# Performance work log

Measured on AMD Instinct MI355X. Metric: run time of the kernel, lower is better.

The kernel has to match this reference:

```python
import jax, jax.numpy as jnp
import numpy as np

B, SQ, SKV, E, H = 4, 2048, 2048, 1024, 16
HD = E // H  # 64


def stablemax(x):
    # StableMax: s(x) = x+1 if x>=0 else 1/(1-x), normalized along last axis
    s = jnp.where(x >= 0, x + 1.0, 1.0 / (1.0 - x))
    return s / jnp.sum(s, axis=-1, keepdims=True)


def setup_inputs() -> dict:
    key = jax.random.key(0)
    ks = jax.random.split(key, 6)
    scale = 1.0 / np.sqrt(E)
    return {
        "query": jax.random.normal(ks[0], (B, SQ, E), jnp.float32),
        "key_value": jax.random.normal(ks[1], (B, SKV, E), jnp.float32),
        "Wq": jax.random.normal(ks[2], (E, E), jnp.float32) * scale,
        "bq": jnp.zeros((E,), jnp.float32),
        "Wk": jax.random.normal(ks[3], (E, E), jnp.float32) * scale,
        "bk": jnp.zeros((E,), jnp.float32),
        "Wv": jax.random.normal(ks[4], (E, E), jnp.float32) * scale,
        "bv": jnp.zeros((E,), jnp.float32),
        "Wo": jax.random.normal(ks[5], (E, E), jnp.float32) * scale,
        "bo": jnp.zeros((E,), jnp.float32),
    }


def reference(query, key_value, Wq, bq, Wk, bk, Wv, bv, Wo, bo):
    b = query.shape[0]
    # linear projections (torch Linear: x @ W^T + b)
    q = query @ Wq.T + bq
    k = key_value @ Wk.T + bk
    v = key_value @ Wv.T + bv
    # [B, H, S, HD]
    q = q.reshape(b, -1, H, HD).transpose(0, 2, 1, 3)
    k = k.reshape(b, -1, H, HD).transpose(0, 2, 1, 3)
    v = v.reshape(b, -1, H, HD).transpose(0, 2, 1, 3)
    scores = jnp.einsum("bhqd,bhkd->bhqk", q, k) / np.sqrt(HD).astype(np.float32)
    attn = stablemax(scores)  # dropout is identity in eval mode
    context = jnp.einsum("bhqk,bhkd->bhqd", attn, v)
    context = context.transpose(0, 2, 1, 3).reshape(b, -1, E)
    return context @ Wo.T + bo
```

## Files before the change

kernel.cpp:

```cpp
#include <hip/hip_runtime.h>

typedef __bf16 bf16;
typedef __bf16 bf16x8 __attribute__((ext_vector_type(8)));
typedef __bf16 bf16x4 __attribute__((ext_vector_type(4)));
typedef _Float16 f16;
typedef _Float16 f16x2 __attribute__((ext_vector_type(2)));
typedef _Float16 f16x4 __attribute__((ext_vector_type(4)));
typedef _Float16 f16x8 __attribute__((ext_vector_type(8)));
typedef float f32x4 __attribute__((ext_vector_type(4)));

__device__ __forceinline__ f32x4 mfma_qk(bf16x8 a, bf16x8 b, f32x4 c) {
    return __builtin_amdgcn_mfma_f32_16x16x32_bf16(a, b, c, 0, 0, 0);
}
__device__ __forceinline__ f32x4 mfma_pv32(f16x8 a, f16x8 b, f32x4 c) {
    return __builtin_amdgcn_mfma_f32_16x16x32_f16(a, b, c, 0, 0, 0);
}

#define GLOAD_LDS16(gp, lp)                                                    \
    __builtin_amdgcn_global_load_lds(                                          \
        (const __attribute__((address_space(1))) unsigned int*)(gp),           \
        (__attribute__((address_space(3))) unsigned int*)(lp), 16, 0, 0)

__global__ __launch_bounds__(256) void cast_inputs(
    const float* __restrict__ w0, const float* __restrict__ w1,
    const float* __restrict__ w2, const float* __restrict__ w3,
    const float* __restrict__ kv, const float* __restrict__ q,
    bf16* __restrict__ Wb, bf16* __restrict__ KVa, bf16* __restrict__ Qb) {
    long i4 = (long)blockIdx.x * 256 + threadIdx.x;
    const float* src;
    bf16* dst;
    long loc;
    if (i4 < 1048576) {
        int which = (int)(i4 >> 18);
        loc = (i4 & 262143) << 2;
        src = which == 0 ? w0 : which == 1 ? w1 : which == 2 ? w2 : w3;
        dst = Wb + ((long)which << 20);
    } else if (i4 < 3145728) {
        loc = (i4 - 1048576) << 2;
        src = kv; dst = KVa;
    } else {
        loc = (i4 - 3145728) << 2;
        src = q; dst = Qb;
    }
    float4 f = *(const float4*)(src + loc);
    bf16x4 o;
    o[0] = (bf16)f.x; o[1] = (bf16)f.y; o[2] = (bf16)f.z; o[3] = (bf16)f.w;
    *(bf16x4*)(dst + loc) = o;
}

__device__ __forceinline__ void gemm_core(
    const bf16* __restrict__ A, const bf16* __restrict__ Wt,
    const float* __restrict__ bias, void* __restrict__ Yv,
    const int om, bf16* smem, const int n0, const int m0) {
    constexpr int Kd = 1024, Nd = 1024;
    constexpr int TP = 132;
    bf16* As = smem;
    bf16* Bs = smem + 8192;
    const int tid = threadIdx.x;
    const int wid = tid >> 6, lane = tid & 63;
    const int l16 = lane & 15, quad = lane >> 4;
    const int mh = (wid >> 1) * 64, nh = (wid & 1) * 64;

    f32x4 acc[4][4];
#pragma unroll
    for (int i = 0; i < 4; ++i)
#pragma unroll
        for (int j = 0; j < 4; ++j) acc[i][j] = (f32x4){0.f, 0.f, 0.f, 0.f};

    for (int k0 = 0; k0 < Kd; k0 += 64) {
#pragma unroll
        for (int j = 0; j < 4; ++j) {
            const int s = j * 256 + tid;
            const int r = s >> 3, c8 = (s & 7) ^ (r & 7);
            GLOAD_LDS16(A + (long)(m0 + r) * Kd + k0 + c8 * 8, &As[s * 8]);
            GLOAD_LDS16(Wt + (long)(n0 + r) * Kd + k0 + c8 * 8, &Bs[s * 8]);
        }
        __syncthreads();
#pragma unroll
        for (int kc = 0; kc < 2; ++kc) {
            bf16x8 af[4], bq[4];
#pragma unroll
            for (int i = 0; i < 4; ++i) {
                const int row = mh + i * 16 + l16;
                af[i] = *(const bf16x8*)&As[(row * 8 + ((kc * 4 + quad) ^ (row & 7))) * 8];
            }
#pragma unroll
            for (int i = 0; i < 4; ++i) {
                const int row = nh + i * 16 + l16;
                bq[i] = *(const bf16x8*)&Bs[(row * 8 + ((kc * 4 + quad) ^ (row & 7))) * 8];
            }
#pragma unroll
            for (int i = 0; i < 4; ++i)
#pragma unroll
                for (int j = 0; j < 4; ++j)
                    acc[i][j] = mfma_qk(af[i], bq[j], acc[i][j]);
        }
        __syncthreads();
    }

    if (om == 2) {
#pragma unroll
        for (int j = 0; j < 4; ++j) {
            const int col = nh + j * 16 + l16;
            const float bv = bias[n0 + col];
#pragma unroll
            for (int i = 0; i < 4; ++i)
#pragma unroll
                for (int p = 0; p < 2; ++p) {
                    f16x2 pk2;
                    pk2[0] = (f16)(acc[i][j][p * 2 + 0] + bv);
                    pk2[1] = (f16)(acc[i][j][p * 2 + 1] + bv);
                    *(f16x2*)&smem[col * TP + mh + i * 16 + quad * 4 + p * 2] = pk2;
                }
        }
        __syncthreads();
        const int b_ = m0 >> 11, skv0 = m0 & 2047;
        const int rowc = tid & 15;
        const int B32 = (rowc >> 2) * 32, g4 = (rowc & 3) * 4;
        const f16* sm = (const f16*)smem;
#pragma unroll
        for (int c = 0; c < 8; ++c) {
            const int col = (tid >> 4) + c * 16;
            const int colg = n0 + col;
            f16x4 lo = *(const f16x4*)&sm[col * TP + B32 + g4];
            f16x4 hi = *(const f16x4*)&sm[col * TP + B32 + 16 + g4];
            f16x8 v = __builtin_shufflevector(lo, hi, 0, 1, 2, 3, 4, 5, 6, 7);
            const long base = ((long)((b_ * 16 + (colg >> 6)) * 64 + (colg & 63))) << 11;
            *(f16x8*)((f16*)Yv + base + skv0 + rowc * 8) = v;
        }
    } else {
#pragma unroll
        for (int j = 0; j < 4; ++j) {
            const int col = n0 + nh + j * 16 + l16;
            const float bv = bias[col];
#pragma unroll
            for (int i = 0; i < 4; ++i)
#pragma unroll
                for (int r = 0; r < 4; ++r) {
                    int row = m0 + mh + i * 16 + quad * 4 + r;
                    float v = acc[i][j][r] + bv;
                    if (om == 1)
                        ((float*)Yv)[(long)row * Nd + col] = v;
                    else
                        ((bf16*)Yv)[(long)row * Nd + col] = (bf16)v;
                }
        }
    }
}

__global__ __launch_bounds__(256) void proj_qkv(
    const bf16* __restrict__ Qb, const bf16* __restrict__ KVa,
    const bf16* __restrict__ Wb,
    const float* __restrict__ bq, const float* __restrict__ bk,
    const float* __restrict__ bv,
    bf16* __restrict__ Qw, bf16* __restrict__ Kw, f16* __restrict__ Vt) {
    __shared__ __align__(16) bf16 smem[16896];
    const int lin = blockIdx.x + (blockIdx.y << 3) + (blockIdx.z << 9);
    const int nid = (lin & 7) * 192 + (lin >> 3);
    const int z = nid >> 9, rem = nid & 511;
    const int n0 = (rem & 7) << 7, m0 = (rem >> 3) << 7;
    if (z == 0)
        gemm_core(Qb, Wb, bq, Qw, 0, smem, n0, m0);
    else if (z == 1)
        gemm_core(KVa, Wb + (1l << 20), bk, Kw, 0, smem, n0, m0);
    else
        gemm_core(KVa, Wb + (2l << 20), bv, Vt, 2, smem, n0, m0);
}

__global__ __launch_bounds__(256) void gemm_o(
    const bf16* __restrict__ Cw, const bf16* __restrict__ Wo,
    const float* __restrict__ bo, float* __restrict__ out) {
    __shared__ __align__(16) bf16 smem[16896];
    const int lin = blockIdx.x + (blockIdx.y << 3);
    const int nid = (lin & 7) * 64 + (lin >> 3);
    gemm_core(Cw, Wo, bo, out, 1, smem, (nid & 7) << 7, (nid >> 3) << 7);
}

__global__ __launch_bounds__(256) void attn_kernel(
    const bf16* __restrict__ Q, const bf16* __restrict__ K,
    const f16* __restrict__ Vt, bf16* __restrict__ C) {
    constexpr int E = 1024, S = 2048, KVB = 64;
    __shared__ __align__(16) char smem_raw[32768];
    bf16* Ks0 = (bf16*)smem_raw;
    bf16* Ks1 = (bf16*)(smem_raw + 8192);
    f16* Vt0 = (f16*)(smem_raw + 16384);
    f16* Vt1 = (f16*)(smem_raw + 24576);

    const int tid = threadIdx.x;
    const int wid = tid >> 6, lane = tid & 63;
    const int l16 = lane & 15, quad = lane >> 4;
    const int lin = blockIdx.x + (blockIdx.y << 4) + (blockIdx.z << 8);
    const int nid = (lin & 7) * 128 + (lin >> 3);
    const int qt = nid & 15, h = (nid >> 4) & 15, b = nid >> 8;

    const long q0 = (long)b * S + qt * 128;
    const bf16* Qg = Q + q0 * E + h * 64;
    const bf16* Kg = K + (long)b * S * E + h * 64;
    const f16* Vg = Vt + ((long)(b * 16 + h) << 17);

    bf16x8 qf[2][2];
#pragma unroll
    for (int mt = 0; mt < 2; ++mt)
#pragma unroll
        for (int kc = 0; kc < 2; ++kc)
            qf[mt][kc] = *(const bf16x8*)(Qg + (long)(wid * 32 + mt * 16 + l16) * E + kc * 32 + quad * 8);

    f16x8 ones8;
#pragma unroll
    for (int j = 0; j < 8; ++j) ones8[j] = (f16)1.0f;

    f32x4 ctx[2][4];
    f32x4 dacc[2];
#pragma unroll
    for (int mt = 0; mt < 2; ++mt) {
        dacc[mt] = (f32x4){0.f, 0.f, 0.f, 0.f};
#pragma unroll
        for (int dt = 0; dt < 4; ++dt) ctx[mt][dt] = (f32x4){0.f, 0.f, 0.f, 0.f};
    }

    auto stage = [&](int kv0, bf16* Kd, f16* Vd) {
#pragma unroll
        for (int j = 0; j < 2; ++j) {
            const int s = j * 256 + tid;
            const int r = s >> 3, c8 = (s & 7) ^ (r & 7);
            GLOAD_LDS16(Kg + (long)(kv0 + r) * E + c8 * 8, &Kd[s * 8]);
        }
#pragma unroll
        for (int j = 0; j < 2; ++j) {
            const int s = j * 256 + tid;
            const int r = s >> 3, c8 = (s & 7) ^ (r & 7);
            GLOAD_LDS16(Vg + (long)r * S + kv0 + c8 * 8, &Vd[s * 8]);
        }
    };

    auto compute = [&](const bf16* Kc, const f16* Vc) {
#pragma unroll
        for (int kvp = 0; kvp < 2; ++kvp) {
            f32x4 sacc[2][2];
#pragma unroll
            for (int sh = 0; sh < 2; ++sh) {
                const int rk = kvp * 32 + sh * 16 + l16, rb = rk & 7;
                bf16x8 kf0 = *(const bf16x8*)&Kc[(rk * 8 + (quad ^ rb)) * 8];
                bf16x8 kf1 = *(const bf16x8*)&Kc[(rk * 8 + ((quad + 4) ^ rb)) * 8];
                __builtin_amdgcn_s_setprio(1);
#pragma unroll
                for (int mt = 0; mt < 2; ++mt) {
                    f32x4 t = mfma_qk(kf0, qf[mt][0], (f32x4){0.f, 0.f, 0.f, 0.f});
                    sacc[sh][mt] = mfma_qk(kf1, qf[mt][1], t);
                }
                __builtin_amdgcn_s_setprio(0);
            }
            f16x8 pp[2];
#pragma unroll
            for (int mt = 0; mt < 2; ++mt)
#pragma unroll
                for (int sh = 0; sh < 2; ++sh)
#pragma unroll
                    for (int r = 0; r < 4; ++r) {
                        float x = sacc[sh][mt][r];
                        float u = __builtin_fmaf(__builtin_fabsf(x), 0.125f, 1.0f);
                        float sv = (x >= 0.f) ? u : __builtin_amdgcn_rcpf(u);
                        pp[mt][sh * 4 + r] = (f16)sv;
                    }
            __builtin_amdgcn_s_setprio(1);
            dacc[0] = mfma_pv32(ones8, pp[0], dacc[0]);
            dacc[1] = mfma_pv32(ones8, pp[1], dacc[1]);
            __builtin_amdgcn_s_setprio(0);
            const int cL = 4 * kvp + quad;
#pragma unroll
            for (int dt = 0; dt < 4; ++dt) {
                const int rv = dt * 16 + l16;
                f16x8 vf = *(const f16x8*)&Vc[(rv * 8 + (cL ^ (rv & 7))) * 8];
                __builtin_amdgcn_s_setprio(1);
#pragma unroll
                for (int mt = 0; mt < 2; ++mt)
                    ctx[mt][dt] = mfma_pv32(vf, pp[mt], ctx[mt][dt]);
                __builtin_amdgcn_s_setprio(0);
            }
        }
    };

    stage(0, Ks0, Vt0);
#pragma unroll 1
    for (int t = 0; t < 31; ++t) {
        const int sel = t & 1;
        stage((t + 1) * KVB, sel ? Ks0 : Ks1, sel ? Vt0 : Vt1);
        asm volatile("s_waitcnt vmcnt(4)\ns_barrier" ::: "memory");
        compute(sel ? Ks1 : Ks0, sel ? Vt1 : Vt0);
        asm volatile("s_waitcnt lgkmcnt(0)\ns_barrier" ::: "memory");
    }
    asm volatile("s_waitcnt vmcnt(0)\ns_barrier" ::: "memory");
    compute(Ks1, Vt1);
    __syncthreads();

    float scl[2];
#pragma unroll
    for (int mt = 0; mt < 2; ++mt) scl[mt] = __builtin_amdgcn_rcpf(dacc[mt][0]);

    bf16* Os = (bf16*)smem_raw;
#pragma unroll
    for (int mt = 0; mt < 2; ++mt)
#pragma unroll
        for (int dt = 0; dt < 4; ++dt) {
            bf16x4 o;
#pragma unroll
            for (int r = 0; r < 4; ++r) o[r] = (bf16)(ctx[mt][dt][r] * scl[mt]);
            *(bf16x4*)&Os[(wid * 32 + mt * 16 + l16) * 68 + dt * 16 + quad * 4] = o;
        }
    __syncthreads();
    {
        const int r = tid >> 1, c = (tid & 1) * 32;
        bf16* cp = C + (q0 + r) * E + h * 64 + c;
#pragma unroll
        for (int j = 0; j < 4; ++j)
            *(bf16x8*)(cp + j * 8) = *(const bf16x8*)&Os[r * 68 + c + j * 8];
    }
}

extern "C" void kernel_launch(void* const* d_in, const int* in_sizes, int n_in,
                              void* d_out, int out_size, void* d_ws, size_t ws_size,
                              hipStream_t stream) {
    const float* query = (const float*)d_in[0];
    const float* keyv  = (const float*)d_in[1];
    const float* Wq = (const float*)d_in[2];
    const float* bq = (const float*)d_in[3];
    const float* Wk = (const float*)d_in[4];
    const float* bk = (const float*)d_in[5];
    const float* Wv = (const float*)d_in[6];
    const float* bv = (const float*)d_in[7];
    const float* Wo = (const float*)d_in[8];
    const float* bo = (const float*)d_in[9];

    char* ws = (char*)d_ws;
    bf16* Wb  = (bf16*)ws;
    bf16* KVa = (bf16*)(ws + (8l << 20));
    bf16* Qb  = (bf16*)(ws + (24l << 20));
    bf16* Qw  = (bf16*)(ws + (40l << 20));
    f16*  Vt  = (f16*)(ws + (56l << 20));
    bf16* Kw  = (bf16*)d_out;
    bf16* Cw  = KVa;

    cast_inputs<<<20480, 256, 0, stream>>>(Wq, Wk, Wv, Wo, keyv, query, Wb, KVa, Qb);

    proj_qkv<<<dim3(8, 64, 3), 256, 0, stream>>>(Qb, KVa, Wb, bq, bk, bv, Qw, Kw, Vt);

    attn_kernel<<<dim3(16, 16, 4), 256, 0, stream>>>(Qw, Kw, Vt, Cw);

    gemm_o<<<dim3(8, 64), 256, 0, stream>>>(Cw, Wb + (3l << 20), bo, (float*)d_out);
}
```

Baseline: 329.5 us.

## Triple-buffer 32-row KV tiles in attention and fold score scale into Wq

The attention main loop changes from double-buffered 64-row K/V tiles to a triple-buffered ring of 32-row tiles. Each stage issues one 16-byte load per thread for K and one for V, and LDS addresses are precomputed per buffer. Only one barrier per step is kept, and each load can be in flight across two compute steps. The 1/sqrt(HD) scale is folded into Wq and bq when casting, which removes the per-score multiply, and the f16 conversion uses packed round-toward-zero conversion. The risks are more barriers per KV element and a slight numerical change from RTZ rounding and the pre-scaled bf16 Wq.

Measured after the change: 312.9 us. -5.1%, faster.

```diff
diff --git a/kernel.cpp b/kernel.cpp
--- a/kernel.cpp
+++ b/kernel.cpp
@@ -7,6 +7,7 @@
 typedef _Float16 f16x2 __attribute__((ext_vector_type(2)));
 typedef _Float16 f16x4 __attribute__((ext_vector_type(4)));
 typedef _Float16 f16x8 __attribute__((ext_vector_type(8)));
+typedef __fp16 h16x2 __attribute__((ext_vector_type(2)));
 typedef float f32x4 __attribute__((ext_vector_type(4)));
 
 __device__ __forceinline__ f32x4 mfma_qk(bf16x8 a, bf16x8 b, f32x4 c) {
@@ -14,6 +15,10 @@
 }
 __device__ __forceinline__ f32x4 mfma_pv32(f16x8 a, f16x8 b, f32x4 c) {
     return __builtin_amdgcn_mfma_f32_16x16x32_f16(a, b, c, 0, 0, 0);
+}
+__device__ __forceinline__ f16x2 pkrtz(float a, float b) {
+    h16x2 r = __builtin_amdgcn_cvt_pkrtz(a, b);
+    return __builtin_bit_cast(f16x2, r);
 }
 
 #define GLOAD_LDS16(gp, lp)                                                    \
@@ -30,11 +35,13 @@
     const float* src;
     bf16* dst;
     long loc;
+    float sc = 1.0f;
     if (i4 < 1048576) {
         int which = (int)(i4 >> 18);
         loc = (i4 & 262143) << 2;
         src = which == 0 ? w0 : which == 1 ? w1 : which == 2 ? w2 : w3;
         dst = Wb + ((long)which << 20);
+        if (which == 0) sc = 0.125f;
     } else if (i4 < 3145728) {
         loc = (i4 - 1048576) << 2;
         src = kv; dst = KVa;
@@ -44,14 +51,15 @@
     }
     float4 f = *(const float4*)(src + loc);
     bf16x4 o;
-    o[0] = (bf16)f.x; o[1] = (bf16)f.y; o[2] = (bf16)f.z; o[3] = (bf16)f.w;
+    o[0] = (bf16)(f.x * sc); o[1] = (bf16)(f.y * sc);
+    o[2] = (bf16)(f.z * sc); o[3] = (bf16)(f.w * sc);
     *(bf16x4*)(dst + loc) = o;
 }
 
 __device__ __forceinline__ void gemm_core(
     const bf16* __restrict__ A, const bf16* __restrict__ Wt,
     const float* __restrict__ bias, void* __restrict__ Yv,
-    const int om, bf16* smem, const int n0, const int m0) {
+    const int om, bf16* smem, const int n0, const int m0, const float bsc) {
     constexpr int Kd = 1024, Nd = 1024;
     constexpr int TP = 132;
     bf16* As = smem;
@@ -102,7 +110,7 @@
 #pragma unroll
         for (int j = 0; j < 4; ++j) {
             const int col = nh + j * 16 + l16;
-            const float bv = bias[n0 + col];
+            const float bv = bias[n0 + col] * bsc;
 #pragma unroll
             for (int i = 0; i < 4; ++i)
 #pragma unroll
@@ -132,7 +140,7 @@
 #pragma unroll
         for (int j = 0; j < 4; ++j) {
             const int col = n0 + nh + j * 16 + l16;
-            const float bv = bias[col];
+            const float bv = bias[col] * bsc;
 #pragma unroll
             for (int i = 0; i < 4; ++i)
 #pragma unroll
@@ -160,11 +168,11 @@
     const int z = nid >> 9, rem = nid & 511;
     const int n0 = (rem & 7) << 7, m0 = (rem >> 3) << 7;
     if (z == 0)
-        gemm_core(Qb, Wb, bq, Qw, 0, smem, n0, m0);
+        gemm_core(Qb, Wb, bq, Qw, 0, smem, n0, m0, 0.125f);
     else if (z == 1)
-        gemm_core(KVa, Wb + (1l << 20), bk, Kw, 0, smem, n0, m0);
+        gemm_core(KVa, Wb + (1l << 20), bk, Kw, 0, smem, n0, m0, 1.0f);
     else
-        gemm_core(KVa, Wb + (2l << 20), bv, Vt, 2, smem, n0, m0);
+        gemm_core(KVa, Wb + (2l << 20), bv, Vt, 2, smem, n0, m0, 1.0f);
 }
 
 __global__ __launch_bounds__(256) void gemm_o(
@@ -173,22 +181,22 @@
     __shared__ __align__(16) bf16 smem[16896];
     const int lin = blockIdx.x + (blockIdx.y << 3);
     const int nid = (lin & 7) * 64 + (lin >> 3);
-    gemm_core(Cw, Wo, bo, out, 1, smem, (nid & 7) << 7, (nid >> 3) << 7);
-}
+    gemm_core(Cw, Wo, bo, out, 1, smem, (nid & 7) << 7, (nid >> 3) << 7, 1.0f);
+}
+
+#define PWAIT2 asm volatile("s_waitcnt vmcnt(2) lgkmcnt(0)\ns_barrier" ::: "memory")
+#define PWAIT0 asm volatile("s_waitcnt vmcnt(0) lgkmcnt(0)\ns_barrier" ::: "memory")
 
 __global__ __launch_bounds__(256) void attn_kernel(
     const bf16* __restrict__ Q, const bf16* __restrict__ K,
     const f16* __restrict__ Vt, bf16* __restrict__ C) {
-    constexpr int E = 1024, S = 2048, KVB = 64;
-    __shared__ __align__(16) char smem_raw[32768];
-    bf16* Ks0 = (bf16*)smem_raw;
-    bf16* Ks1 = (bf16*)(smem_raw + 8192);
-    f16* Vt0 = (f16*)(smem_raw + 16384);
-    f16* Vt1 = (f16*)(smem_raw + 24576);
+    constexpr int E = 1024, S = 2048;
+    __shared__ __align__(16) char smem_raw[24576];
 
     const int tid = threadIdx.x;
     const int wid = tid >> 6, lane = tid & 63;
     const int l16 = lane & 15, quad = lane >> 4;
+    const int l7 = l16 & 7, l3 = l16 & 3;
     const int lin = blockIdx.x + (blockIdx.y << 4) + (blockIdx.z << 8);
     const int nid = (lin & 7) * 128 + (lin >> 3);
     const int qt = nid & 15, h = (nid >> 4) & 15, b = nid >> 8;
@@ -204,6 +212,18 @@
 #pragma unroll
         for (int kc = 0; kc < 2; ++kc)
             qf[mt][kc] = *(const bf16x8*)(Qg + (long)(wid * 32 + mt * 16 + l16) * E + kc * 32 + quad * 8);
+    asm volatile("s_waitcnt vmcnt(0)" ::: "memory");
+
+    const bf16* Ksrc = Kg + (long)(tid >> 3) * E + (((tid & 7) ^ ((tid >> 3) & 7)) * 8);
+    const f16* Vsrc = Vg + (long)(tid >> 2) * S + (((tid & 3) ^ ((tid >> 2) & 3)) * 8);
+
+    int ka0[3], ka1[3], va[3];
+#pragma unroll
+    for (int i = 0; i < 3; ++i) {
+        ka0[i] = i * 8192 + l16 * 128 + ((quad ^ l7) << 4);
+        ka1[i] = i * 8192 + l16 * 128 + (((quad + 4) ^ l7) << 4);
+        va[i]  = i * 8192 + 4096 + l16 * 64 + ((quad ^ l3) << 4);
+    }
 
     f16x8 ones8;
 #pragma unroll
@@ -218,79 +238,73 @@
         for (int dt = 0; dt < 4; ++dt) ctx[mt][dt] = (f32x4){0.f, 0.f, 0.f, 0.f};
     }
 
-    auto stage = [&](int kv0, bf16* Kd, f16* Vd) {
-#pragma unroll
-        for (int j = 0; j < 2; ++j) {
-            const int s = j * 256 + tid;
-            const int r = s >> 3, c8 = (s & 7) ^ (r & 7);
-            GLOAD_LDS16(Kg + (long)(kv0 + r) * E + c8 * 8, &Kd[s * 8]);
-        }
-#pragma unroll
-        for (int j = 0; j < 2; ++j) {
-            const int s = j * 256 + tid;
-            const int r = s >> 3, c8 = (s & 7) ^ (r & 7);
-            GLOAD_LDS16(Vg + (long)r * S + kv0 + c8 * 8, &Vd[s * 8]);
-        }
+    auto stage = [&](int kv0, int bi) {
+        GLOAD_LDS16(Ksrc + (long)kv0 * E, smem_raw + bi * 8192 + tid * 16);
+        GLOAD_LDS16(Vsrc + kv0, smem_raw + bi * 8192 + 4096 + tid * 16);
     };
 
-    auto compute = [&](const bf16* Kc, const f16* Vc) {
-#pragma unroll
-        for (int kvp = 0; kvp < 2; ++kvp) {
-            f32x4 sacc[2][2];
-#pragma unroll
-            for (int sh = 0; sh < 2; ++sh) {
-                const int rk = kvp * 32 + sh * 16 + l16, rb = rk & 7;
-                bf16x8 kf0 = *(const bf16x8*)&Kc[(rk * 8 + (quad ^ rb)) * 8];
-                bf16x8 kf1 = *(const bf16x8*)&Kc[(rk * 8 + ((quad + 4) ^ rb)) * 8];
-                __builtin_amdgcn_s_setprio(1);
-#pragma unroll
-                for (int mt = 0; mt < 2; ++mt) {
-                    f32x4 t = mfma_qk(kf0, qf[mt][0], (f32x4){0.f, 0.f, 0.f, 0.f});
-                    sacc[sh][mt] = mfma_qk(kf1, qf[mt][1], t);
+    auto compute = [&](int bi) {
+        f32x4 sacc[2][2];
+#pragma unroll
+        for (int sh = 0; sh < 2; ++sh) {
+            bf16x8 kf0 = *(const bf16x8*)(smem_raw + ka0[bi] + sh * 2048);
+            bf16x8 kf1 = *(const bf16x8*)(smem_raw + ka1[bi] + sh * 2048);
+            __builtin_amdgcn_s_setprio(1);
+#pragma unroll
+            for (int mt = 0; mt < 2; ++mt) {
+                f32x4 t = mfma_qk(kf0, qf[mt][0], (f32x4){0.f, 0.f, 0.f, 0.f});
+                sacc[sh][mt] = mfma_qk(kf1, qf[mt][1], t);
+            }
+            __builtin_amdgcn_s_setprio(0);
+        }
+        f16x8 pp[2];
+#pragma unroll
+        for (int mt = 0; mt < 2; ++mt) {
+            float sv[8];
+#pragma unroll
+            for (int sh = 0; sh < 2; ++sh)
+#pragma unroll
+                for (int r = 0; r < 4; ++r) {
+                    float x = sacc[sh][mt][r];
+                    float u = __builtin_fabsf(x) + 1.0f;
+                    sv[sh * 4 + r] = (x >= 0.f) ? u : __builtin_amdgcn_rcpf(u);
                 }
-                __builtin_amdgcn_s_setprio(0);
-            }
-            f16x8 pp[2];
+            f16x2 w0 = pkrtz(sv[0], sv[1]);
+            f16x2 w1 = pkrtz(sv[2], sv[3]);
+            f16x2 w2 = pkrtz(sv[4], sv[5]);
+            f16x2 w3 = pkrtz(sv[6], sv[7]);
+            f16x4 lo = __builtin_shufflevector(w0, w1, 0, 1, 2, 3);
+            f16x4 hi = __builtin_shufflevector(w2, w3, 0, 1, 2, 3);
+            pp[mt] = __builtin_shufflevector(lo, hi, 0, 1, 2, 3, 4, 5, 6, 7);
+        }
+        __builtin_amdgcn_s_setprio(1);
+        dacc[0] = mfma_pv32(ones8, pp[0], dacc[0]);
+        dacc[1] = mfma_pv32(ones8, pp[1], dacc[1]);
+        __builtin_amdgcn_s_setprio(0);
+#pragma unroll
+        for (int dt = 0; dt < 4; ++dt) {
+            f16x8 vf = *(const f16x8*)(smem_raw + va[bi] + dt * 1024);
+            __builtin_amdgcn_s_setprio(1);
 #pragma unroll
             for (int mt = 0; mt < 2; ++mt)
-#pragma unroll
-                for (int sh = 0; sh < 2; ++sh)
-#pragma unroll
-                    for (int r = 0; r < 4; ++r) {
-                        float x = sacc[sh][mt][r];
-                        float u = __builtin_fmaf(__builtin_fabsf(x), 0.125f, 1.0f);
-                        float sv = (x >= 0.f) ? u : __builtin_amdgcn_rcpf(u);
-                        pp[mt][sh * 4 + r] = (f16)sv;
-                    }
-            __builtin_amdgcn_s_setprio(1);
-            dacc[0] = mfma_pv32(ones8, pp[0], dacc[0]);
-            dacc[1] = mfma_pv32(ones8, pp[1], dacc[1]);
+                ctx[mt][dt] = mfma_pv32(vf, pp[mt], ctx[mt][dt]);
             __builtin_amdgcn_s_setprio(0);
-            const int cL = 4 * kvp + quad;
-#pragma unroll
-            for (int dt = 0; dt < 4; ++dt) {
-                const int rv = dt * 16 + l16;
-                f16x8 vf = *(const f16x8*)&Vc[(rv * 8 + (cL ^ (rv & 7))) * 8];
-                __builtin_amdgcn_s_setprio(1);
-#pragma unroll
-                for (int mt = 0; mt < 2; ++mt)
-                    ctx[mt][dt] = mfma_pv32(vf, pp[mt], ctx[mt][dt]);
-                __builtin_amdgcn_s_setprio(0);
-            }
         }
     };
 
-    stage(0, Ks0, Vt0);
+    stage(0, 0);
+    stage(32, 1);
+    int kv = 64;
 #pragma unroll 1
-    for (int t = 0; t < 31; ++t) {
-        const int sel = t & 1;
-        stage((t + 1) * KVB, sel ? Ks0 : Ks1, sel ? Vt0 : Vt1);
-        asm volatile("s_waitcnt vmcnt(4)\ns_barrier" ::: "memory");
-        compute(sel ? Ks1 : Ks0, sel ? Vt1 : Vt0);
-        asm volatile("s_waitcnt lgkmcnt(0)\ns_barrier" ::: "memory");
-    }
-    asm volatile("s_waitcnt vmcnt(0)\ns_barrier" ::: "memory");
-    compute(Ks1, Vt1);
+    for (int it = 0; it < 20; ++it) {
+        PWAIT2; stage(kv, 2); compute(0); kv += 32;
+        PWAIT2; stage(kv, 0); compute(1); kv += 32;
+        PWAIT2; stage(kv, 1); compute(2); kv += 32;
+    }
+    PWAIT2; stage(kv, 2); compute(0);
+    PWAIT2; stage(kv + 32, 0); compute(1);
+    PWAIT2; compute(2);
+    PWAIT0; compute(0);
     __syncthreads();
 
     float scl[2];
```
